# Kernel tuning notes

Hardware: AMD Instinct MI355X
Metric: run time of the kernel (lower is better)

## Reference

```python
import jax, jax.numpy as jnp
import numpy as np
from jax import lax

HIDDEN = 128
HEADS = 2
SR = 4
EPS = 1e-5


def _rope(x, fr, fi):
    # x: (B, h, S, d) ; fr, fi: (S, d//2) broadcast as (1,1,S,c)
    B, H, S, D = x.shape
    x2 = x.reshape(B, H, S, D // 2, 2)
    xr, xi = x2[..., 0], x2[..., 1]
    fr = fr[None, None, :, :]
    fi = fi[None, None, :, :]
    out_r = xr * fr - xi * fi
    out_i = xr * fi + xi * fr
    return jnp.stack([out_r, out_i], axis=-1).reshape(B, H, S, D)


def _layernorm(x, g, b):
    mu = jnp.mean(x, axis=-1, keepdims=True)
    var = jnp.mean(jnp.square(x - mu), axis=-1, keepdims=True)
    return (x - mu) * lax.rsqrt(var + EPS) * g + b


def setup_inputs() -> dict:
    key = jax.random.key(0)
    ks = jax.random.split(key, 12)
    B, S, C = 2, 16384, HIDDEN
    s = 0.02
    return {
        "hidden_states": jax.random.normal(ks[0], (B, S, C), jnp.float32),
        "freqs_cis": jax.random.normal(ks[1], (S, C // HEADS // 2, 2), jnp.float32),
        "Wq": jax.random.normal(ks[2], (C, C), jnp.float32) * s,
        "bq": jnp.zeros((C,), jnp.float32),
        "Wk": jax.random.normal(ks[3], (C, C), jnp.float32) * s,
        "bk": jnp.zeros((C,), jnp.float32),
        "Wv": jax.random.normal(ks[4], (C, C), jnp.float32) * s,
        "bv": jnp.zeros((C,), jnp.float32),
        "W_sr": jax.random.normal(ks[5], (C, C, SR, SR), jnp.float32) * s,  # (O,I,kh,kw)
        "b_sr": jnp.zeros((C,), jnp.float32),
        "ln_g": jnp.ones((C,), jnp.float32),
        "ln_b": jnp.zeros((C,), jnp.float32),
        "height": 128,
        "width": 128,
    }


def reference(hidden_states, freqs_cis, Wq, bq, Wk, bk, Wv, bv, W_sr, b_sr, ln_g, ln_b, height, width):
    B, S, C = hidden_states.shape
    h, d = HEADS, C // HEADS
    c = d // 2

    # query projection on full-resolution tokens
    q = (hidden_states @ Wq.T + bq).reshape(B, S, h, d).transpose(0, 2, 1, 3)  # (B,h,S,d)

    # sequence reduction: conv stride=kernel=SR on (B,C,H,W), then layernorm
    x_img = hidden_states.transpose(0, 2, 1).reshape(B, C, height, width)
    xr = lax.conv_general_dilated(x_img, W_sr, window_strides=(SR, SR), padding="VALID")
    xr = xr + b_sr[None, :, None, None]
    Sk = (height // SR) * (width // SR)
    xr = xr.reshape(B, C, Sk).transpose(0, 2, 1)  # (B, S', C)
    xr = _layernorm(xr, ln_g, ln_b)

    k = (xr @ Wk.T + bk).reshape(B, Sk, h, d).transpose(0, 2, 1, 3)
    v = (xr @ Wv.T + bv).reshape(B, Sk, h, d).transpose(0, 2, 1, 3)

    # RoPE: queries use full freqs; keys use sr-pooled (block-mean) freqs
    fr, fi = freqs_cis[..., 0], freqs_cis[..., 1]  # (S, c)
    q = _rope(q, fr, fi)

    fr_img = fr.reshape(height // SR, SR, width // SR, SR, c).mean(axis=(1, 3))
    fi_img = fi.reshape(height // SR, SR, width // SR, SR, c).mean(axis=(1, 3))
    fr_k = fr_img.reshape(Sk, c)
    fi_k = fi_img.reshape(Sk, c)
    k = _rope(k, fr_k, fi_k)

    scores = jnp.einsum("bhqd,bhkd->bhqk", q, k) / jnp.sqrt(jnp.float32(d))
    probs = jax.nn.softmax(scores, axis=-1)
    ctx = jnp.einsum("bhqk,bhkd->bhqd", probs, v)
    return ctx.transpose(0, 2, 1, 3).reshape(B, S, C)
```

## Files before the change

### kernel.cpp

```cpp
#include <hip/hip_runtime.h>
#include <math.h>

#define B_   2
#define S_   16384
#define SK_  1024
#define IMW_ 128
#define EPS_ 1e-5f

typedef __attribute__((ext_vector_type(8))) short short8v;
typedef __attribute__((ext_vector_type(4))) short short4v;
typedef __attribute__((ext_vector_type(4))) float f32x4;

__device__ __forceinline__ ushort f2bfu(float x) {
    uint u = __float_as_uint(x);
    u += 0x7fffu + ((u >> 16) & 1u);
    return (ushort)(u >> 16);
}
__device__ __forceinline__ uint cvtpk(float a, float b) {
    uint r;
    asm("v_cvt_pk_bf16_f32 %0, %1, %2" : "=v"(r) : "v"(a), "v"(b));
    return r;
}
__device__ __forceinline__ short8v pack8(float4 a, float4 b) {
    union { uint4 u; short8v s; } c;
    c.u = make_uint4(cvtpk(a.x, a.y), cvtpk(a.z, a.w), cvtpk(b.x, b.y), cvtpk(b.z, b.w));
    return c.s;
}

__global__ __launch_bounds__(256) void k_prep(
    const float* __restrict__ Wsr, const float* __restrict__ Wq,
    const float* __restrict__ Wk,  const float* __restrict__ Wv,
    const float* __restrict__ fc,
    ushort* __restrict__ Wsrb, ushort* __restrict__ Wqb,
    ushort* __restrict__ Wkb,  ushort* __restrict__ Wvb,
    float* __restrict__ frk, float* __restrict__ fik)
{
    const int blk = blockIdx.x, t = threadIdx.x;
    if (blk < 64) {
        int i = blk * 256 + t;
        int co = i >> 7, ci = i & 127;
        const float* src = Wsr + (size_t)i * 16;
        float4 v0 = *(const float4*)(src);
        float4 v1 = *(const float4*)(src + 4);
        float4 v2 = *(const float4*)(src + 8);
        float4 v3 = *(const float4*)(src + 12);
        float vv[16] = {v0.x, v0.y, v0.z, v0.w, v1.x, v1.y, v1.z, v1.w,
                        v2.x, v2.y, v2.z, v2.w, v3.x, v3.y, v3.z, v3.w};
        ushort* dst = Wsrb + (size_t)co * 2048 + ci;
        #pragma unroll
        for (int tap = 0; tap < 16; ++tap) dst[tap * 128] = f2bfu(vv[tap]);
    } else if (blk < 88) {
        int seg = (blk - 64) >> 3;
        const float* src = (seg == 0) ? Wq : (seg == 1) ? Wk : Wv;
        ushort* dst = (seg == 0) ? Wqb : (seg == 1) ? Wkb : Wvb;
        int i = ((blk - 64) & 7) * 2048 + t * 8;
        float4 a = *(const float4*)(src + i);
        float4 b = *(const float4*)(src + i + 4);
        *(uint4*)(dst + i) = make_uint4(cvtpk(a.x, a.y), cvtpk(a.z, a.w),
                                        cvtpk(b.x, b.y), cvtpk(b.z, b.w));
    } else {
        int idx = (blk - 88) * 256 + t;
        int c = idx & 31, kk = idx >> 5;
        int y = kk >> 5, x = kk & 31;
        float sr = 0.f, si = 0.f;
        #pragma unroll
        for (int i1 = 0; i1 < 4; ++i1)
            #pragma unroll
            for (int i3 = 0; i3 < 4; ++i3) {
                int s = (4 * y + i1) * IMW_ + 4 * x + i3;
                sr += fc[s * 64 + 2 * c];
                si += fc[s * 64 + 2 * c + 1];
            }
        frk[idx] = sr * 0.0625f;
        fik[idx] = si * 0.0625f;
    }
}

__global__ __launch_bounds__(512) void k_conv(
    const float* __restrict__ hid, const ushort* __restrict__ Wsrb,
    float* __restrict__ partial)
{
    const int t = threadIdx.x;
    const int lane = t & 63, w = t >> 6;
    const int g = lane >> 4, ln = lane & 15;
    const int b = blockIdx.x >> 6, pt = blockIdx.x & 63;
    const int pos = pt * 16 + ln;
    const int y = pos >> 5, x = pos & 31;

    f32x4 acc[8];
    #pragma unroll
    for (int mt = 0; mt < 8; ++mt)
        #pragma unroll
        for (int r = 0; r < 4; ++r) acc[mt][r] = 0.f;

    #pragma unroll
    for (int st = 0; st < 8; ++st) {
        const int tap = 2 * w + (st >> 2);
        const int ci0 = (st & 3) * 32;
        const int ky = tap >> 2, kx = tap & 3;
        const float* hp = hid + ((size_t)b * S_ + (4 * y + ky) * IMW_ + 4 * x + kx) * 128 + ci0 + 8 * g;
        short8v xf = pack8(*(const float4*)hp, *(const float4*)(hp + 4));
        #pragma unroll
        for (int mt = 0; mt < 8; ++mt) {
            short8v wf = *(const short8v*)(Wsrb + (size_t)(16 * mt + ln) * 2048 + tap * 128 + ci0 + 8 * g);
            acc[mt] = __builtin_amdgcn_mfma_f32_16x16x32_bf16(wf, xf, acc[mt], 0, 0, 0);
        }
    }
    float* dst = partial + ((size_t)w * 2048 + b * 1024 + pos) * 128 + 4 * g;
    #pragma unroll
    for (int mt = 0; mt < 8; ++mt)
        *(float4*)(dst + 16 * mt) = make_float4(acc[mt][0], acc[mt][1], acc[mt][2], acc[mt][3]);
}

__global__ __launch_bounds__(256) void k_lnkv(
    const float* __restrict__ partial, const float* __restrict__ bsr,
    const float* __restrict__ lng, const float* __restrict__ lnb,
    const float* __restrict__ FRK, const float* __restrict__ FIK,
    const ushort* __restrict__ Wkb, const ushort* __restrict__ Wvb,
    const float* __restrict__ bk, const float* __restrict__ bv,
    ushort* __restrict__ Kb, ushort* __restrict__ VTb)
{
    __shared__ ushort sXb[16][128];
    const int t = threadIdx.x;
    const int lane = t & 63, w = t >> 6;
    const int g = lane >> 4, ln = lane & 15;
    const int b = blockIdx.x >> 6;
    const int row0 = blockIdx.x * 16;
    const int pos0 = (blockIdx.x & 63) * 16;

    {
        const int row = t >> 4, j0 = (t & 15) * 8;
        float4 b0 = *(const float4*)(bsr + j0);
        float4 b1 = *(const float4*)(bsr + j0 + 4);
        float v[8] = {b0.x, b0.y, b0.z, b0.w, b1.x, b1.y, b1.z, b1.w};
        #pragma unroll
        for (int s = 0; s < 8; ++s) {
            const float* pp = partial + ((size_t)s * 2048 + row0 + row) * 128 + j0;
            float4 a = *(const float4*)pp;
            float4 c = *(const float4*)(pp + 4);
            v[0] += a.x; v[1] += a.y; v[2] += a.z; v[3] += a.w;
            v[4] += c.x; v[5] += c.y; v[6] += c.z; v[7] += c.w;
        }
        float s = v[0] + v[1] + v[2] + v[3] + v[4] + v[5] + v[6] + v[7];
        #pragma unroll
        for (int m = 1; m < 16; m <<= 1) s += __shfl_xor(s, m, 64);
        float mu = s * (1.0f / 128.0f);
        float d[8], vs = 0.f;
        #pragma unroll
        for (int j = 0; j < 8; ++j) { d[j] = v[j] - mu; vs += d[j] * d[j]; }
        #pragma unroll
        for (int m = 1; m < 16; m <<= 1) vs += __shfl_xor(vs, m, 64);
        float rstd = rsqrtf(vs * (1.0f / 128.0f) + EPS_);
        float4 g0 = *(const float4*)(lng + j0);
        float4 g1 = *(const float4*)(lng + j0 + 4);
        float4 c0 = *(const float4*)(lnb + j0);
        float4 c1 = *(const float4*)(lnb + j0 + 4);
        float o[8];
        o[0] = d[0] * rstd * g0.x + c0.x; o[1] = d[1] * rstd * g0.y + c0.y;
        o[2] = d[2] * rstd * g0.z + c0.z; o[3] = d[3] * rstd * g0.w + c0.w;
        o[4] = d[4] * rstd * g1.x + c1.x; o[5] = d[5] * rstd * g1.y + c1.y;
        o[6] = d[6] * rstd * g1.z + c1.z; o[7] = d[7] * rstd * g1.w + c1.w;
        *(uint4*)&sXb[row][j0 ^ ((row & 7) << 3)] =
            make_uint4(cvtpk(o[0], o[1]), cvtpk(o[2], o[3]),
                       cvtpk(o[4], o[5]), cvtpk(o[6], o[7]));
    }
    __syncthreads();

    short8v xn[4];
    #pragma unroll
    for (int ks = 0; ks < 4; ++ks)
        xn[ks] = *(const short8v*)&sXb[ln][(32 * ks + 8 * g) ^ ((ln & 7) << 3)];

    const int h = w & 1;
    const ushort* Wb = (w < 2) ? Wkb : Wvb;
    f32x4 acc2[4];
    #pragma unroll
    for (int mt = 0; mt < 4; ++mt)
        #pragma unroll
        for (int r = 0; r < 4; ++r) acc2[mt][r] = 0.f;
    #pragma unroll
    for (int mt = 0; mt < 4; ++mt)
        #pragma unroll
        for (int ks = 0; ks < 4; ++ks) {
            short8v wf = *(const short8v*)(Wb + (size_t)(64 * h + 16 * mt + ln) * 128 + 32 * ks + 8 * g);
            acc2[mt] = __builtin_amdgcn_mfma_f32_16x16x32_bf16(wf, xn[ks], acc2[mt], 0, 0, 0);
        }

    const int posg = pos0 + ln;
    const int bh = b * 2 + h;
    if (w < 2) {
        #pragma unroll
        for (int mt = 0; mt < 4; ++mt) {
            int col0 = 16 * mt + 4 * g;
            float4 bkv = *(const float4*)(bk + 64 * h + col0);
            float a0 = acc2[mt][0] + bkv.x, a1 = acc2[mt][1] + bkv.y;
            float a2 = acc2[mt][2] + bkv.z, a3 = acc2[mt][3] + bkv.w;
            float2 frv = *(const float2*)(FRK + (size_t)posg * 32 + (col0 >> 1));
            float2 fiv = *(const float2*)(FIK + (size_t)posg * 32 + (col0 >> 1));
            float o0 = a0 * frv.x - a1 * fiv.x;
            float o1 = a0 * fiv.x + a1 * frv.x;
            float o2 = a2 * frv.y - a3 * fiv.y;
            float o3 = a2 * fiv.y + a3 * frv.y;
            *(uint2*)(Kb + ((size_t)bh * SK_ + posg) * 64 + col0) =
                make_uint2(cvtpk(o0, o1), cvtpk(o2, o3));
        }
    } else {
        #pragma unroll
        for (int mt = 0; mt < 4; ++mt) {
            int col0 = 16 * mt + 4 * g;
            float4 bvv = *(const float4*)(bv + 64 * h + col0);
            #pragma unroll
            for (int r = 0; r < 4; ++r)
                VTb[((size_t)bh * 64 + col0 + r) * SK_ + posg] =
                    f2bfu(acc2[mt][r] + (&bvv.x)[r]);
        }
    }
}

__global__ __launch_bounds__(256) void k_attn(
    const float* __restrict__ hid, const ushort* __restrict__ Wqb,
    const float* __restrict__ bq, const float* __restrict__ fc,
    const ushort* __restrict__ Kb, const ushort* __restrict__ VTb,
    float* __restrict__ out)
{
    __shared__ ushort sK[64][72];
    __shared__ ushort sVT[64][72];

    const int t = threadIdx.x;
    const int lane = t & 63, w = t >> 6;
    const int g = lane >> 4, ln = lane & 15;
    const int sbid = (blockIdx.x & 7) * 128 + (blockIdx.x >> 3);
    const int bh = sbid >> 8;
    const int q0b = (sbid & 255) * 64;
    const int b = bh >> 1, h = bh & 1;

    ushort* sQt = &sK[0][0];

    {
        f32x4 qa[4];
        #pragma unroll
        for (int mt = 0; mt < 4; ++mt)
            #pragma unroll
            for (int r = 0; r < 4; ++r) qa[mt][r] = 0.f;

        #pragma unroll
        for (int ks = 0; ks < 4; ++ks) {
            const float* hp = hid + ((size_t)b * S_ + q0b + w * 16 + ln) * 128 + 32 * ks + 8 * g;
            short8v xf = pack8(*(const float4*)hp, *(const float4*)(hp + 4));
            #pragma unroll
            for (int mt = 0; mt < 4; ++mt) {
                short8v wf = *(const short8v*)(Wqb + (size_t)(64 * h + 16 * mt + ln) * 128 + 32 * ks + 8 * g);
                qa[mt] = __builtin_amdgcn_mfma_f32_16x16x32_bf16(wf, xf, qa[mt], 0, 0, 0);
            }
        }
        const float scale = 0.18033688011112042f;
        const int pos = q0b + w * 16 + ln;
        #pragma unroll
        for (int mt = 0; mt < 4; ++mt) {
            int col0 = 16 * mt + 4 * g;
            float4 fv = *(const float4*)(fc + (size_t)pos * 64 + col0);
            float4 bqv = *(const float4*)(bq + 64 * h + col0);
            float a0 = qa[mt][0] + bqv.x, a1 = qa[mt][1] + bqv.y;
            float a2 = qa[mt][2] + bqv.z, a3 = qa[mt][3] + bqv.w;
            float o0 = (a0 * fv.x - a1 * fv.y) * scale;
            float o1 = (a0 * fv.y + a1 * fv.x) * scale;
            float o2 = (a2 * fv.z - a3 * fv.w) * scale;
            float o3 = (a2 * fv.w + a3 * fv.z) * scale;
            *(uint2*)&sQt[(w * 16 + ln) * 72 + col0] = make_uint2(cvtpk(o0, o1), cvtpk(o2, o3));
        }
    }
    short8v qf[2];
    #pragma unroll
    for (int ks = 0; ks < 2; ++ks)
        qf[ks] = *(const short8v*)&sQt[(w * 16 + ln) * 72 + 32 * ks + 8 * g];
    __syncthreads();

    const int f0 = t, f1 = t + 256;
    const size_t kOff0 = (size_t)((f0 >> 3) * 64 + (f0 & 7) * 8);
    const size_t kOff1 = (size_t)((f1 >> 3) * 64 + (f1 & 7) * 8);
    const size_t vOff0 = (size_t)((f0 >> 3) * SK_ + (f0 & 7) * 8);
    const size_t vOff1 = (size_t)((f1 >> 3) * SK_ + (f1 & 7) * 8);
    const ushort* kgBase = Kb  + (size_t)bh * SK_ * 64;
    const ushort* vgBase = VTb + (size_t)bh * 64 * SK_;

    f32x4 ctx[4];
    #pragma unroll
    for (int dt = 0; dt < 4; ++dt)
        #pragma unroll
        for (int r = 0; r < 4; ++r) ctx[dt][r] = 0.f;
    float l_run = 0.f;

    uint4 kr0 = *(const uint4*)(kgBase + kOff0);
    uint4 kr1 = *(const uint4*)(kgBase + kOff1);
    uint4 vr0 = *(const uint4*)(vgBase + vOff0);
    uint4 vr1 = *(const uint4*)(vgBase + vOff1);

    for (int ch = 0; ch < 16; ++ch) {
        __syncthreads();
        *(uint4*)&sK[f0 >> 3][(f0 & 7) * 8]  = kr0;
        *(uint4*)&sK[f1 >> 3][(f1 & 7) * 8]  = kr1;
        *(uint4*)&sVT[f0 >> 3][(f0 & 7) * 8] = vr0;
        *(uint4*)&sVT[f1 >> 3][(f1 & 7) * 8] = vr1;
        __syncthreads();
        if (ch < 15) {
            kr0 = *(const uint4*)(kgBase + (ch + 1) * 4096 + kOff0);
            kr1 = *(const uint4*)(kgBase + (ch + 1) * 4096 + kOff1);
            vr0 = *(const uint4*)(vgBase + (ch + 1) * 64 + vOff0);
            vr1 = *(const uint4*)(vgBase + (ch + 1) * 64 + vOff1);
        }

        f32x4 sc[4];
        #pragma unroll
        for (int kvt = 0; kvt < 4; ++kvt)
            #pragma unroll
            for (int r = 0; r < 4; ++r) sc[kvt][r] = 0.f;
        #pragma unroll
        for (int ks = 0; ks < 2; ++ks)
            #pragma unroll
            for (int kvt = 0; kvt < 4; ++kvt) {
                short8v kf = *(const short8v*)&sK[16 * kvt + ln][32 * ks + 8 * g];
                sc[kvt] = __builtin_amdgcn_mfma_f32_16x16x32_bf16(kf, qf[ks], sc[kvt], 0, 0, 0);
            }

        #pragma unroll
        for (int kvt = 0; kvt < 4; ++kvt)
            #pragma unroll
            for (int r = 0; r < 4; ++r) {
                float ev = __builtin_amdgcn_exp2f(sc[kvt][r]);
                sc[kvt][r] = ev;
                l_run += ev;
            }

        #pragma unroll
        for (int ks2 = 0; ks2 < 2; ++ks2) {
            union { uint4 u; short8v s; } pf;
            pf.u.x = cvtpk(sc[2 * ks2][0],     sc[2 * ks2][1]);
            pf.u.y = cvtpk(sc[2 * ks2][2],     sc[2 * ks2][3]);
            pf.u.z = cvtpk(sc[2 * ks2 + 1][0], sc[2 * ks2 + 1][1]);
            pf.u.w = cvtpk(sc[2 * ks2 + 1][2], sc[2 * ks2 + 1][3]);
            #pragma unroll
            for (int dt = 0; dt < 4; ++dt) {
                const int dd = 16 * dt + ln;
                short4v va = *(const short4v*)&sVT[dd][32 * ks2 + 4 * g];
                short4v vb = *(const short4v*)&sVT[dd][32 * ks2 + 16 + 4 * g];
                short8v vf = __builtin_shufflevector(va, vb, 0, 1, 2, 3, 4, 5, 6, 7);
                ctx[dt] = __builtin_amdgcn_mfma_f32_16x16x32_bf16(pf.s, vf, ctx[dt], 0, 0, 0);
            }
        }
    }

    float l = l_run;
    l += __shfl_xor(l, 16, 64);
    l += __shfl_xor(l, 32, 64);
    float inv = 1.0f / l;
    #pragma unroll
    for (int r = 0; r < 4; ++r) {
        float ir = __shfl(inv, 4 * g + r, 64);
        int q = q0b + w * 16 + 4 * g + r;
        float* dst = out + ((size_t)b * S_ + q) * 128 + h * 64;
        #pragma unroll
        for (int dt = 0; dt < 4; ++dt)
            dst[16 * dt + ln] = ctx[dt][r] * ir;
    }
}

extern "C" void kernel_launch(void* const* d_in, const int* in_sizes, int n_in,
                              void* d_out, int out_size, void* d_ws, size_t ws_size,
                              hipStream_t stream) {
    const float* hid = (const float*)d_in[0];
    const float* fc  = (const float*)d_in[1];
    const float* Wq  = (const float*)d_in[2];
    const float* bq  = (const float*)d_in[3];
    const float* Wk  = (const float*)d_in[4];
    const float* bk  = (const float*)d_in[5];
    const float* Wv  = (const float*)d_in[6];
    const float* bv  = (const float*)d_in[7];
    const float* Wsr = (const float*)d_in[8];
    const float* bsr = (const float*)d_in[9];
    const float* lng = (const float*)d_in[10];
    const float* lnb = (const float*)d_in[11];
    float* out = (float*)d_out;

    float* ws = (float*)d_ws;
    float*  partial = ws;
    float*  FRK  = ws + 2097152;
    float*  FIK  = ws + 2129920;
    ushort* Wsrb = (ushort*)(ws + 2162688);
    ushort* Kb   = (ushort*)(ws + 2293760);
    ushort* VTb  = (ushort*)(ws + 2424832);
    ushort* Wqb  = (ushort*)(ws + 2555904);
    ushort* Wkb  = (ushort*)(ws + 2564096);
    ushort* Wvb  = (ushort*)(ws + 2572288);

    k_prep<<<216, 256, 0, stream>>>(Wsr, Wq, Wk, Wv, fc,
                                    Wsrb, Wqb, Wkb, Wvb, FRK, FIK);
    k_conv<<<128, 512, 0, stream>>>(hid, Wsrb, partial);
    k_lnkv<<<128, 256, 0, stream>>>(partial, bsr, lng, lnb, FRK, FIK,
                                    Wkb, Wvb, bk, bv, Kb, VTb);
    k_attn<<<1024, 256, 0, stream>>>(hid, Wqb, bq, fc, Kb, VTb, out);
}
```

Before: 78.61 us.

## Double-buffer K/V shared tiles with XOR swizzle and pre-permuted V loads

Replaces the padded single-buffer K/V shared-memory tiles with double-buffered, XOR-swizzled 64x64 tiles. This allows one barrier per chunk instead of two, with global loads issued two chunks ahead. V is loaded in a pre-permuted order so the PV MFMA operand becomes a single 16-byte LDS read instead of two 8-byte reads plus a shuffle. The aim is fewer barrier stalls and bank conflicts, at the cost of more LDS and more registers held for prefetch.

```diff
diff --git a/kernel.cpp b/kernel.cpp
--- a/kernel.cpp
+++ b/kernel.cpp
@@ -223,8 +223,8 @@
     const ushort* __restrict__ Kb, const ushort* __restrict__ VTb,
     float* __restrict__ out)
 {
-    __shared__ ushort sK[64][72];
-    __shared__ ushort sVT[64][72];
+    __shared__ ushort sK[2][64][64];
+    __shared__ ushort sV[2][64][64];
 
     const int t = threadIdx.x;
     const int lane = t & 63, w = t >> 6;
@@ -234,7 +234,7 @@
     const int q0b = (sbid & 255) * 64;
     const int b = bh >> 1, h = bh & 1;
 
-    ushort* sQt = &sK[0][0];
+    char* sQt = (char*)&sK[0][0][0];
 
     {
         f32x4 qa[4];
@@ -254,7 +254,8 @@
             }
         }
         const float scale = 0.18033688011112042f;
-        const int pos = q0b + w * 16 + ln;
+        const int r = w * 16 + ln;
+        const int pos = q0b + r;
         #pragma unroll
         for (int mt = 0; mt < 4; ++mt) {
             int col0 = 16 * mt + 4 * g;
@@ -266,22 +267,46 @@
             float o1 = (a0 * fv.y + a1 * fv.x) * scale;
             float o2 = (a2 * fv.z - a3 * fv.w) * scale;
             float o3 = (a2 * fv.w + a3 * fv.z) * scale;
-            *(uint2*)&sQt[(w * 16 + ln) * 72 + col0] = make_uint2(cvtpk(o0, o1), cvtpk(o2, o3));
+            int cb = ((col0 >> 3) ^ (r & 7));
+            *(uint2*)(sQt + r * 128 + cb * 16 + (g & 1) * 8) =
+                make_uint2(cvtpk(o0, o1), cvtpk(o2, o3));
         }
     }
     short8v qf[2];
     #pragma unroll
-    for (int ks = 0; ks < 2; ++ks)
-        qf[ks] = *(const short8v*)&sQt[(w * 16 + ln) * 72 + 32 * ks + 8 * g];
+    for (int ks = 0; ks < 2; ++ks) {
+        const int r = w * 16 + ln;
+        qf[ks] = *(const short8v*)(sQt + r * 128 + (((4 * ks + g) ^ (r & 7)) * 16));
+    }
     __syncthreads();
 
-    const int f0 = t, f1 = t + 256;
-    const size_t kOff0 = (size_t)((f0 >> 3) * 64 + (f0 & 7) * 8);
-    const size_t kOff1 = (size_t)((f1 >> 3) * 64 + (f1 & 7) * 8);
-    const size_t vOff0 = (size_t)((f0 >> 3) * SK_ + (f0 & 7) * 8);
-    const size_t vOff1 = (size_t)((f1 >> 3) * SK_ + (f1 & 7) * 8);
-    const ushort* kgBase = Kb  + (size_t)bh * SK_ * 64;
-    const ushort* vgBase = VTb + (size_t)bh * 64 * SK_;
+    const int r0 = t >> 3, m0 = t & 7;
+    const int r1 = r0 + 32;
+    const int vA = 32 * (m0 >> 2) + 4 * (m0 & 3);
+    const ushort* kgB = Kb  + (size_t)bh * SK_ * 64;
+    const ushort* vgB = VTb + (size_t)bh * 64 * SK_;
+
+    uint4 kb0, kb1, vb0, vb1;
+    auto loadCh = [&](int ch) {
+        const ushort* kp = kgB + (size_t)ch * 4096;
+        kb0 = *(const uint4*)(kp + r0 * 64 + m0 * 8);
+        kb1 = *(const uint4*)(kp + r1 * 64 + m0 * 8);
+        const ushort* vp = vgB + ch * 64;
+        uint2 a0 = *(const uint2*)(vp + (size_t)r0 * SK_ + vA);
+        uint2 b0 = *(const uint2*)(vp + (size_t)r0 * SK_ + vA + 16);
+        uint2 a1 = *(const uint2*)(vp + (size_t)r1 * SK_ + vA);
+        uint2 b1 = *(const uint2*)(vp + (size_t)r1 * SK_ + vA + 16);
+        vb0 = make_uint4(a0.x, a0.y, b0.x, b0.y);
+        vb1 = make_uint4(a1.x, a1.y, b1.x, b1.y);
+    };
+    auto writeBuf = [&](int p) {
+        char* kd = (char*)&sK[p][0][0];
+        char* vd = (char*)&sV[p][0][0];
+        *(uint4*)(kd + r0 * 128 + ((m0 ^ (r0 & 7)) * 16)) = kb0;
+        *(uint4*)(kd + r1 * 128 + ((m0 ^ (r1 & 7)) * 16)) = kb1;
+        *(uint4*)(vd + r0 * 128 + ((m0 ^ (r0 & 7)) * 16)) = vb0;
+        *(uint4*)(vd + r1 * 128 + ((m0 ^ (r1 & 7)) * 16)) = vb1;
+    };
 
     f32x4 ctx[4];
     #pragma unroll
@@ -290,23 +315,16 @@
         for (int r = 0; r < 4; ++r) ctx[dt][r] = 0.f;
     float l_run = 0.f;
 
-    uint4 kr0 = *(const uint4*)(kgBase + kOff0);
-    uint4 kr1 = *(const uint4*)(kgBase + kOff1);
-    uint4 vr0 = *(const uint4*)(vgBase + vOff0);
-    uint4 vr1 = *(const uint4*)(vgBase + vOff1);
+    loadCh(0);
+    writeBuf(0);
+    loadCh(1);
+    __syncthreads();
 
     for (int ch = 0; ch < 16; ++ch) {
-        __syncthreads();
-        *(uint4*)&sK[f0 >> 3][(f0 & 7) * 8]  = kr0;
-        *(uint4*)&sK[f1 >> 3][(f1 & 7) * 8]  = kr1;
-        *(uint4*)&sVT[f0 >> 3][(f0 & 7) * 8] = vr0;
-        *(uint4*)&sVT[f1 >> 3][(f1 & 7) * 8] = vr1;
-        __syncthreads();
+        const int p = ch & 1;
         if (ch < 15) {
-            kr0 = *(const uint4*)(kgBase + (ch + 1) * 4096 + kOff0);
-            kr1 = *(const uint4*)(kgBase + (ch + 1) * 4096 + kOff1);
-            vr0 = *(const uint4*)(vgBase + (ch + 1) * 64 + vOff0);
-            vr1 = *(const uint4*)(vgBase + (ch + 1) * 64 + vOff1);
+            writeBuf(p ^ 1);
+            if (ch < 14) loadCh(ch + 2);
         }
 
         f32x4 sc[4];
@@ -318,7 +336,9 @@
         for (int ks = 0; ks < 2; ++ks)
             #pragma unroll
             for (int kvt = 0; kvt < 4; ++kvt) {
-                short8v kf = *(const short8v*)&sK[16 * kvt + ln][32 * ks + 8 * g];
+                const int r = 16 * kvt + ln;
+                short8v kf = *(const short8v*)((const char*)&sK[p][0][0] +
+                                               r * 128 + (((4 * ks + g) ^ (r & 7)) * 16));
                 sc[kvt] = __builtin_amdgcn_mfma_f32_16x16x32_bf16(kf, qf[ks], sc[kvt], 0, 0, 0);
             }
 
@@ -341,12 +361,13 @@
             #pragma unroll
             for (int dt = 0; dt < 4; ++dt) {
                 const int dd = 16 * dt + ln;
-                short4v va = *(const short4v*)&sVT[dd][32 * ks2 + 4 * g];
-                short4v vb = *(const short4v*)&sVT[dd][32 * ks2 + 16 + 4 * g];
-                short8v vf = __builtin_shufflevector(va, vb, 0, 1, 2, 3, 4, 5, 6, 7);
+                short8v vf = *(const short8v*)((const char*)&sV[p][0][0] +
+                                               dd * 128 + (((4 * ks2 + g) ^ (dd & 7)) * 16));
                 ctx[dt] = __builtin_amdgcn_mfma_f32_16x16x32_bf16(pf.s, vf, ctx[dt], 0, 0, 0);
             }
         }
+
+        __syncthreads();
     }
 
     float l = l_run;
```

New measurement: 78.21 us. No clear change (-0.5%).
